# Optimization experiments

Measured on AMD Instinct MI355X. Metric: run time of the kernel, lower is better.

Reference implementation:

```python
import jax, jax.numpy as jnp
import numpy as np

B, OUT, IN = 1024, 512, 1024

def setup_inputs() -> dict:
    key = jax.random.key(0)
    k1, k2, k3, k4 = jax.random.split(key, 4)
    x = jax.random.uniform(k1, (B, IN), dtype=jnp.float32)            # inputs in [0,1]
    w = jax.random.uniform(k2, (OUT, IN), dtype=jnp.float32)          # centers in [min_input, max_input]=[0,1]
    u = jax.random.uniform(k3, (OUT, IN), dtype=jnp.float32, minval=0.2, maxval=0.7)  # slopes per init
    andor01 = jax.random.randint(k4, (1, OUT), 0, 2).astype(jnp.float32)  # frozen 0/1 mix ('*' mode)
    return {"x": x, "w": w, "u": u, "andor01": andor01}

def reference(x, w, u, andor01):
    # xuw = u * (x[b,None,i] - w[o,i]) ; z[b,o] = sum_i xuw^2 ; y = exp(-z)
    diff = u[None, :, :] * (x[:, None, :] - w[None, :, :])   # [B, OUT, IN]
    z = jnp.sum(diff * diff, axis=-1)                        # [B, OUT]
    y = jnp.exp(-z)                                          # forward of LargeAttractorExp
    # andor == '*': y + andor01 * (1 - 2y)
    return y + andor01 * (1.0 - 2.0 * y)
```

## Files before the change

### kernel.cpp

```cpp
#include <hip/hip_runtime.h>

#define B_SZ   1024
#define OUT_SZ 512
#define IN_SZ  1024

#define MB 32
#define NB 32
#define CH 128
#define NKC (IN_SZ / CH)

typedef __bf16 bf16x8 __attribute__((ext_vector_type(8)));
typedef __bf16 bf16x4 __attribute__((ext_vector_type(4)));
typedef float  f32x4  __attribute__((ext_vector_type(4)));

#define A_IDX(seg, s, f, slot) (((((seg)*4 + (s))*2 + (f))*64 + (slot))*8)
#define B_IDX(seg, s, f, slot) (((((seg)*4 + (s))*2 + (f))*64 + (slot))*8)

__global__ __launch_bounds__(512, 4) void rbf_one(
    const float* __restrict__ x, const float* __restrict__ w,
    const float* __restrict__ u, const float* __restrict__ andor,
    float* __restrict__ out)
{
    __shared__ __bf16 Asm[2 * 4 * 2 * 64 * 8];
    __shared__ __bf16 Bsm[2 * 4 * 2 * 64 * 8];
    __shared__ float  accsm[4 * 64 * 4];
    __shared__ float  r_lds[NB];

    const int t    = threadIdx.x;
    const int lane = t & 63;
    const int wv   = t >> 6;
    const int ks   = wv & 1;
    const int wn   = (wv >> 1) & 1;
    const int wm   = (wv >> 2) & 1;

    const int bid = blockIdx.x;
    const int swz = (bid & 7) * 64 + (bid >> 3);
    const int nT = swz >> 5, mT = swz & 31;
    const int mBase = mT * MB, nBase = nT * NB;

    f32x4 acc = {};
    float rp = 0.f;

    const int row = t >> 4;
    const int k4  = (t & 15) * 4;

    float4 xr[2], ur[2], wr[2];
    auto load_regs = [&](int c) {
        #pragma unroll
        for (int h = 0; h < 2; ++h) {
            const int gk = c * CH + h * 64 + k4;
            xr[h] = *(const float4*)&x[(size_t)(mBase + row) * IN_SZ + gk];
            ur[h] = *(const float4*)&u[(size_t)(nBase + row) * IN_SZ + gk];
            wr[h] = *(const float4*)&w[(size_t)(nBase + row) * IN_SZ + gk];
        }
    };

    auto write_lds = [&]() {
        #pragma unroll
        for (int h = 0; h < 2; ++h) {
            const int kl   = h * 64 + k4;
            const int sW   = kl >> 5;
            const int quad = (kl >> 3) & 3;
            const int j0   = kl & 7;
            const int frag = row >> 4;
            const int slot = quad * 16 + (((row & 15) ^ quad) & 15);
            float xv[4]  = {xr[h].x, xr[h].y, xr[h].z, xr[h].w};
            float uv[4]  = {ur[h].x, ur[h].y, ur[h].z, ur[h].w};
            float wv4[4] = {wr[h].x, wr[h].y, wr[h].z, wr[h].w};
            bf16x4 a0, a1, b0, b1;
            #pragma unroll
            for (int e = 0; e < 4; ++e) {
                float xe = xv[e], ue = uv[e], we = wv4[e];
                float u2 = ue * ue, p = ue * we;
                a0[e] = (__bf16)(xe * xe);
                a1[e] = (__bf16)xe;
                b0[e] = (__bf16)u2;
                b1[e] = (__bf16)(-2.f * u2 * we);
                rp = fmaf(p, p, rp);
            }
            *(bf16x4*)&Asm[A_IDX(0, sW, frag, slot) + j0] = a0;
            *(bf16x4*)&Asm[A_IDX(1, sW, frag, slot) + j0] = a1;
            *(bf16x4*)&Bsm[B_IDX(0, sW, frag, slot) + j0] = b0;
            *(bf16x4*)&Bsm[B_IDX(1, sW, frag, slot) + j0] = b1;
        }
    };

    const int r_quad = lane >> 4;
    const int r_slot = r_quad * 16 + (((lane & 15) ^ r_quad) & 15);

    load_regs(0);
    for (int c = 0; c < NKC; ++c) {
        if (c) __syncthreads();
        write_lds();
        __syncthreads();
        if (c + 1 < NKC) load_regs(c + 1);
        #pragma unroll
        for (int seg = 0; seg < 2; ++seg)
            #pragma unroll
            for (int sh = 0; sh < 2; ++sh) {
                bf16x8 am = *(const bf16x8*)&Asm[A_IDX(seg, ks * 2 + sh, wm, r_slot)];
                bf16x8 bn = *(const bf16x8*)&Bsm[B_IDX(seg, ks * 2 + sh, wn, r_slot)];
                acc = __builtin_amdgcn_mfma_f32_16x16x32_bf16(am, bn, acc, 0, 0, 0);
            }
    }

    rp += __shfl_xor(rp, 1);
    rp += __shfl_xor(rp, 2);
    rp += __shfl_xor(rp, 4);
    rp += __shfl_xor(rp, 8);
    if ((lane & 15) == 0) r_lds[row] = rp;

    __syncthreads();
    if (ks == 1)
        *(f32x4*)&accsm[((wm * 2 + wn) * 64 + lane) * 4] = acc;
    __syncthreads();

    if (ks == 0) {
        f32x4 o4 = *(const f32x4*)&accsm[((wm * 2 + wn) * 64 + lane) * 4];
        const int col = lane & 15, rq = lane >> 4;
        const int b = mBase + wm * 16 + rq * 4;
        const int o = nBase + wn * 16 + col;
        const float rv = r_lds[wn * 16 + col];
        const float a  = andor[o];
        const float cf = 1.f - 2.f * a;
        #pragma unroll
        for (int r = 0; r < 4; ++r) {
            float y = __expf(-(acc[r] + o4[r] + rv));
            out[(size_t)(b + r) * OUT_SZ + o] = fmaf(y, cf, a);
        }
    }
}

extern "C" void kernel_launch(void* const* d_in, const int* in_sizes, int n_in,
                              void* d_out, int out_size, void* d_ws, size_t ws_size,
                              hipStream_t stream) {
    const float* x = (const float*)d_in[0];
    const float* w = (const float*)d_in[1];
    const float* u = (const float*)d_in[2];
    const float* a = (const float*)d_in[3];
    float* out = (float*)d_out;

    rbf_one<<<dim3((B_SZ / MB) * (OUT_SZ / NB)), dim3(512), 0, stream>>>(
        x, w, u, a, out);
}
```

Measured before the change: 73.40 us.

## Double-buffer LDS tiles and prefetch global loads two chunks ahead

Shared-memory A/B tiles become ping-pong buffers, and the register staging holds two chunk sets, so global loads for chunk c+2 are issued while chunk c is computed. Chunk c+1 is written into the other LDS buffer during the same step. This leaves one barrier per iteration instead of two and hides load latency behind MFMA work. In exchange it doubles LDS use and register staging. Indexing the register arrays by the runtime value c&1 could spill to scratch if the loop is not fully unrolled.

```diff
diff --git a/kernel.cpp b/kernel.cpp
--- a/kernel.cpp
+++ b/kernel.cpp
@@ -21,8 +21,8 @@
     const float* __restrict__ u, const float* __restrict__ andor,
     float* __restrict__ out)
 {
-    __shared__ __bf16 Asm[2 * 4 * 2 * 64 * 8];
-    __shared__ __bf16 Bsm[2 * 4 * 2 * 64 * 8];
+    __shared__ __bf16 Asm[2][2 * 4 * 2 * 64 * 8];
+    __shared__ __bf16 Bsm[2][2 * 4 * 2 * 64 * 8];
     __shared__ float  accsm[4 * 64 * 4];
     __shared__ float  r_lds[NB];
 
@@ -44,18 +44,18 @@
     const int row = t >> 4;
     const int k4  = (t & 15) * 4;
 
-    float4 xr[2], ur[2], wr[2];
-    auto load_regs = [&](int c) {
+    float4 xr[2][2], ur[2][2], wr[2][2];
+    auto load_regs = [&](int c, int set) {
         #pragma unroll
         for (int h = 0; h < 2; ++h) {
             const int gk = c * CH + h * 64 + k4;
-            xr[h] = *(const float4*)&x[(size_t)(mBase + row) * IN_SZ + gk];
-            ur[h] = *(const float4*)&u[(size_t)(nBase + row) * IN_SZ + gk];
-            wr[h] = *(const float4*)&w[(size_t)(nBase + row) * IN_SZ + gk];
+            xr[set][h] = *(const float4*)&x[(size_t)(mBase + row) * IN_SZ + gk];
+            ur[set][h] = *(const float4*)&u[(size_t)(nBase + row) * IN_SZ + gk];
+            wr[set][h] = *(const float4*)&w[(size_t)(nBase + row) * IN_SZ + gk];
         }
     };
 
-    auto write_lds = [&]() {
+    auto write_lds = [&](int buf, int set) {
         #pragma unroll
         for (int h = 0; h < 2; ++h) {
             const int kl   = h * 64 + k4;
@@ -64,9 +64,9 @@
             const int j0   = kl & 7;
             const int frag = row >> 4;
             const int slot = quad * 16 + (((row & 15) ^ quad) & 15);
-            float xv[4]  = {xr[h].x, xr[h].y, xr[h].z, xr[h].w};
-            float uv[4]  = {ur[h].x, ur[h].y, ur[h].z, ur[h].w};
-            float wv4[4] = {wr[h].x, wr[h].y, wr[h].z, wr[h].w};
+            float xv[4]  = {xr[set][h].x, xr[set][h].y, xr[set][h].z, xr[set][h].w};
+            float uv[4]  = {ur[set][h].x, ur[set][h].y, ur[set][h].z, ur[set][h].w};
+            float wv4[4] = {wr[set][h].x, wr[set][h].y, wr[set][h].z, wr[set][h].w};
             bf16x4 a0, a1, b0, b1;
             #pragma unroll
             for (int e = 0; e < 4; ++e) {
@@ -78,30 +78,37 @@
                 b1[e] = (__bf16)(-2.f * u2 * we);
                 rp = fmaf(p, p, rp);
             }
-            *(bf16x4*)&Asm[A_IDX(0, sW, frag, slot) + j0] = a0;
-            *(bf16x4*)&Asm[A_IDX(1, sW, frag, slot) + j0] = a1;
-            *(bf16x4*)&Bsm[B_IDX(0, sW, frag, slot) + j0] = b0;
-            *(bf16x4*)&Bsm[B_IDX(1, sW, frag, slot) + j0] = b1;
+            *(bf16x4*)&Asm[buf][A_IDX(0, sW, frag, slot) + j0] = a0;
+            *(bf16x4*)&Asm[buf][A_IDX(1, sW, frag, slot) + j0] = a1;
+            *(bf16x4*)&Bsm[buf][B_IDX(0, sW, frag, slot) + j0] = b0;
+            *(bf16x4*)&Bsm[buf][B_IDX(1, sW, frag, slot) + j0] = b1;
         }
     };
 
     const int r_quad = lane >> 4;
     const int r_slot = r_quad * 16 + (((lane & 15) ^ r_quad) & 15);
 
-    load_regs(0);
-    for (int c = 0; c < NKC; ++c) {
-        if (c) __syncthreads();
-        write_lds();
-        __syncthreads();
-        if (c + 1 < NKC) load_regs(c + 1);
+    auto compute = [&](int buf) {
         #pragma unroll
         for (int seg = 0; seg < 2; ++seg)
             #pragma unroll
             for (int sh = 0; sh < 2; ++sh) {
-                bf16x8 am = *(const bf16x8*)&Asm[A_IDX(seg, ks * 2 + sh, wm, r_slot)];
-                bf16x8 bn = *(const bf16x8*)&Bsm[B_IDX(seg, ks * 2 + sh, wn, r_slot)];
+                bf16x8 am = *(const bf16x8*)&Asm[buf][A_IDX(seg, ks * 2 + sh, wm, r_slot)];
+                bf16x8 bn = *(const bf16x8*)&Bsm[buf][B_IDX(seg, ks * 2 + sh, wn, r_slot)];
                 acc = __builtin_amdgcn_mfma_f32_16x16x32_bf16(am, bn, acc, 0, 0, 0);
             }
+    };
+
+    load_regs(0, 0);
+    write_lds(0, 0);
+    load_regs(1, 1);
+    __syncthreads();
+
+    for (int c = 0; c < NKC; ++c) {
+        if (c + 2 < NKC) load_regs(c + 2, c & 1);
+        compute(c & 1);
+        if (c + 1 < NKC) write_lds((c + 1) & 1, (c + 1) & 1);
+        __syncthreads();
     }
 
     rp += __shfl_xor(rp, 1);
@@ -110,7 +117,6 @@
     rp += __shfl_xor(rp, 8);
     if ((lane & 15) == 0) r_lds[row] = rp;
 
-    __syncthreads();
     if (ks == 1)
         *(f32x4*)&accsm[((wm * 2 + wn) * 64 + lane) * 4] = acc;
     __syncthreads();
```

Result: no change. 73.19 us (-0.3%).
